# Optimization experiments

Hardware: AMD Instinct MI355X
Metric: run time of the kernel (lower is better)

Reference implementation:

```python
import jax, jax.numpy as jnp
import numpy as np

N, E, DIN, DH, DOUT = 100000, 600000, 128, 128, 64


def _glorot(k, shape):
    lim = float(np.sqrt(6.0 / (shape[0] + shape[1])))
    return jax.random.uniform(k, shape, jnp.float32, -lim, lim)


def setup_inputs() -> dict:
    key = jax.random.key(0)
    ks = jax.random.split(key, 12)
    return {
        "x": jax.random.normal(ks[0], (N, DIN), jnp.float32),
        "src": jax.random.randint(ks[1], (E,), 0, N),
        "dst": jax.random.randint(ks[2], (E,), 0, N),
        # layer 0: NGNN_SAGEConv = SAGEConv(in,hid) + fc(hid,hid) + fc2(hid,hid)
        "w_self0": _glorot(ks[3], (DIN, DH)), "b_self0": jnp.zeros((DH,), jnp.float32),
        "w_neigh0": _glorot(ks[4], (DIN, DH)),
        "fc_w": _glorot(ks[5], (DH, DH)), "fc_b": jnp.zeros((DH,), jnp.float32),
        "fc2_w": _glorot(ks[6], (DH, DH)), "fc2_b": jnp.zeros((DH,), jnp.float32),
        # layer 1: SAGEConv(hid,hid)
        "w_self1": _glorot(ks[7], (DH, DH)), "b_self1": jnp.zeros((DH,), jnp.float32),
        "w_neigh1": _glorot(ks[8], (DH, DH)),
        # layer 2: SAGEConv(hid,out)
        "w_self2": _glorot(ks[9], (DH, DOUT)), "b_self2": jnp.zeros((DOUT,), jnp.float32),
        "w_neigh2": _glorot(ks[10], (DH, DOUT)),
    }


def _sage_conv(x, src, dst, w_self, b_self, w_neigh):
    # DGL SAGEConv, aggregator='mean': out = x @ W_self + b + mean_{u->v} x_u @ W_neigh
    agg = jax.ops.segment_sum(x[src], dst, num_segments=N)          # [N, d_in]
    deg = jax.ops.segment_sum(jnp.ones((src.shape[0],), x.dtype), dst, num_segments=N)
    h_neigh = agg / jnp.maximum(deg, 1.0)[:, None]                  # zero-in-degree -> 0
    return x @ w_self + b_self + h_neigh @ w_neigh


def reference(x, src, dst,
              w_self0, b_self0, w_neigh0, fc_w, fc_b, fc2_w, fc2_b,
              w_self1, b_self1, w_neigh1,
              w_self2, b_self2, w_neigh2):
    # layer 0: NGNN_SAGEConv with num_nonl_layers=2, then outer ReLU (dropout: eval = identity)
    h = _sage_conv(x, src, dst, w_self0, b_self0, w_neigh0)
    h = jax.nn.relu(h)
    h = h @ fc_w + fc_b
    h = jax.nn.relu(h)
    h = h @ fc2_w + fc2_b
    h = jax.nn.relu(h)
    # layer 1: SAGEConv + ReLU
    h = _sage_conv(h, src, dst, w_self1, b_self1, w_neigh1)
    h = jax.nn.relu(h)
    # layer 2 (output): SAGEConv, no activation
    return _sage_conv(h, src, dst, w_self2, b_self2, w_neigh2)
```

## Files before the change

kernel.cpp:

```cpp
#include <hip/hip_runtime.h>

#define N_NODES 100000
#define N_EDGES 600000
#define K_DIM   128
#define NPART   ((N_NODES + 255) / 256)

typedef unsigned short ushort_t;
typedef short v8s __attribute__((ext_vector_type(8)));
typedef float v4f __attribute__((ext_vector_type(4)));

__device__ __forceinline__ ushort_t f2b(float f) {
  unsigned u = __builtin_bit_cast(unsigned, f);
  unsigned r = u + 0x7FFFu + ((u >> 16) & 1u);
  return (ushort_t)(r >> 16);
}
__device__ __forceinline__ float b2f(ushort_t h) {
  return __builtin_bit_cast(float, (unsigned)h << 16);
}
__device__ __forceinline__ float blo(unsigned u) {
  return __builtin_bit_cast(float, u << 16);
}
__device__ __forceinline__ float bhi(unsigned u) {
  return __builtin_bit_cast(float, u & 0xFFFF0000u);
}


__global__ void deg_kernel(const int* __restrict__ dst, int* __restrict__ deg) {
  int e = blockIdx.x * blockDim.x + threadIdx.x;
  if (e < N_EDGES) atomicAdd(&deg[dst[e]], 1);
}

__global__ void scan1_kernel(const int* __restrict__ deg, int* __restrict__ excl,
                             int* __restrict__ partials) {
  __shared__ int s[256];
  int t = threadIdx.x, i = blockIdx.x * 256 + t;
  int v = (i < N_NODES) ? deg[i] : 0;
  s[t] = v;
  __syncthreads();
  for (int off = 1; off < 256; off <<= 1) {
    int x = (t >= off) ? s[t - off] : 0;
    __syncthreads();
    s[t] += x;
    __syncthreads();
  }
  if (i < N_NODES) excl[i] = s[t] - v;
  if (t == 255) partials[blockIdx.x] = s[t];
}

__global__ void scan2_kernel(int* __restrict__ partials) {
  __shared__ int s[512];
  int t = threadIdx.x;
  int v = (t < NPART) ? partials[t] : 0;
  s[t] = v;
  __syncthreads();
  for (int off = 1; off < 512; off <<= 1) {
    int x = (t >= off) ? s[t - off] : 0;
    __syncthreads();
    s[t] += x;
    __syncthreads();
  }
  if (t < NPART) partials[t] = s[t] - v;
}

__global__ void scan3_kernel(const int* __restrict__ excl, const int* __restrict__ partials,
                             const int* __restrict__ deg, int* __restrict__ row_ptr,
                             int* __restrict__ cursor, float* __restrict__ inv_deg) {
  int i = blockIdx.x * blockDim.x + threadIdx.x;
  if (i < N_NODES) {
    int rp = excl[i] + partials[i >> 8];
    row_ptr[i] = rp;
    cursor[i] = rp;
    inv_deg[i] = 1.0f / (float)(deg[i] > 1 ? deg[i] : 1);
  } else if (i == N_NODES) {
    row_ptr[N_NODES] = N_EDGES;
  }
}

__global__ void fill_kernel(const int* __restrict__ src, const int* __restrict__ dst,
                            int* __restrict__ cursor, int* __restrict__ ssrc) {
  int e = blockIdx.x * blockDim.x + threadIdx.x;
  if (e < N_EDGES) {
    int p = atomicAdd(&cursor[dst[e]], 1);
    ssrc[p] = src[e];
  }
}


__global__ void cast_kernel(const float* __restrict__ X, ushort_t* __restrict__ Xb) {
  int i = (blockIdx.x * 256 + threadIdx.x) * 4;
  if (i >= N_NODES * K_DIM) return;
  float4 v = *(const float4*)(X + i);
  ushort4 h;
  h.x = f2b(v.x); h.y = f2b(v.y); h.z = f2b(v.z); h.w = f2b(v.w);
  *(ushort4*)(Xb + i) = h;
}

__global__ void swizzle_all_kernel(
    const float* __restrict__ w0, const float* __restrict__ w1,
    const float* __restrict__ w2, const float* __restrict__ w3,
    const float* __restrict__ w4, const float* __restrict__ w5,
    const float* __restrict__ w6, const float* __restrict__ w7,
    ushort_t* __restrict__ s0, ushort_t* __restrict__ s1,
    ushort_t* __restrict__ s2, ushort_t* __restrict__ s3,
    ushort_t* __restrict__ s4, ushort_t* __restrict__ s5,
    ushort_t* __restrict__ s6, ushort_t* __restrict__ s7) {
  const int z = blockIdx.z;
  const float* W;
  ushort_t* S;
  int dout = 128;
  switch (z) {
    case 0: W = w0; S = s0; break;
    case 1: W = w1; S = s1; break;
    case 2: W = w2; S = s2; break;
    case 3: W = w3; S = s3; break;
    case 4: W = w4; S = s4; break;
    case 5: W = w5; S = s5; break;
    case 6: W = w6; S = s6; dout = 64; break;
    default: W = w7; S = s7; dout = 64; break;
  }
  int t = blockIdx.x * 256 + threadIdx.x;
  if (t >= K_DIM * dout) return;
  int k = t / dout, n = t % dout;
  S[(k >> 3) * (dout * 8) + n * 8 + (k & 7)] = f2b(W[t]);
}


__global__ __launch_bounds__(256, 8) void agg_kernel(
    const ushort_t* __restrict__ Hh,
    const int* __restrict__ row_ptr, const int* __restrict__ ssrc,
    const float* __restrict__ inv_deg, ushort_t* __restrict__ Ah) {
  const int tid = threadIdx.x;
  const int c0  = (tid & 7) * 16;
  const int r   = tid >> 3;
  const int v   = blockIdx.x * 32 + r;
  if (v >= N_NODES) return;

  float a[16];
  #pragma unroll
  for (int i = 0; i < 16; ++i) a[i] = 0.f;

  const int beg = row_ptr[v], end = row_ptr[v + 1];
  int e = beg;
  for (; e + 2 <= end; e += 2) {
    const size_t r0 = (size_t)ssrc[e] * K_DIM + c0;
    const size_t r1 = (size_t)ssrc[e + 1] * K_DIM + c0;
    const uint4 p0 = *(const uint4*)(Hh + r0);
    const uint4 p1 = *(const uint4*)(Hh + r0 + 8);
    const uint4 q0 = *(const uint4*)(Hh + r1);
    const uint4 q1 = *(const uint4*)(Hh + r1 + 8);
    a[ 0] += blo(p0.x) + blo(q0.x);  a[ 1] += bhi(p0.x) + bhi(q0.x);
    a[ 2] += blo(p0.y) + blo(q0.y);  a[ 3] += bhi(p0.y) + bhi(q0.y);
    a[ 4] += blo(p0.z) + blo(q0.z);  a[ 5] += bhi(p0.z) + bhi(q0.z);
    a[ 6] += blo(p0.w) + blo(q0.w);  a[ 7] += bhi(p0.w) + bhi(q0.w);
    a[ 8] += blo(p1.x) + blo(q1.x);  a[ 9] += bhi(p1.x) + bhi(q1.x);
    a[10] += blo(p1.y) + blo(q1.y);  a[11] += bhi(p1.y) + bhi(q1.y);
    a[12] += blo(p1.z) + blo(q1.z);  a[13] += bhi(p1.z) + bhi(q1.z);
    a[14] += blo(p1.w) + blo(q1.w);  a[15] += bhi(p1.w) + bhi(q1.w);
  }
  if (e < end) {
    const size_t r0 = (size_t)ssrc[e] * K_DIM + c0;
    const uint4 p0 = *(const uint4*)(Hh + r0);
    const uint4 p1 = *(const uint4*)(Hh + r0 + 8);
    a[ 0] += blo(p0.x);  a[ 1] += bhi(p0.x);
    a[ 2] += blo(p0.y);  a[ 3] += bhi(p0.y);
    a[ 4] += blo(p0.z);  a[ 5] += bhi(p0.z);
    a[ 6] += blo(p0.w);  a[ 7] += bhi(p0.w);
    a[ 8] += blo(p1.x);  a[ 9] += bhi(p1.x);
    a[10] += blo(p1.y);  a[11] += bhi(p1.y);
    a[12] += blo(p1.z);  a[13] += bhi(p1.z);
    a[14] += blo(p1.w);  a[15] += bhi(p1.w);
  }
  const float sc = inv_deg[v];
  const size_t wo = (size_t)v * K_DIM + c0;
  #pragma unroll
  for (int g = 0; g < 4; ++g) {
    ushort4 oh;
    oh.x = f2b(a[4 * g + 0] * sc);
    oh.y = f2b(a[4 * g + 1] * sc);
    oh.z = f2b(a[4 * g + 2] * sc);
    oh.w = f2b(a[4 * g + 3] * sc);
    *(ushort4*)(Ah + wo + 4 * g) = oh;
  }
}


template <int DOUT_FULL, bool TWO, bool RELU, bool BF16_OUT>
__global__ __launch_bounds__(256, 4) void mfma_gemm_kernel(
    const ushort_t* __restrict__ A1, const ushort_t* __restrict__ A2,
    const ushort_t* __restrict__ W1sw, const ushort_t* __restrict__ W2sw,
    const float* __restrict__ bias,
    ushort_t* __restrict__ Obf, float* __restrict__ Ofp) {
  constexpr int COLT = 64;
  constexpr int NT   = COLT / 16;
  constexpr int SWN  = (K_DIM / 8) * COLT * 8;
  __shared__ ushort_t sW[SWN];

  const int tid  = threadIdx.x;
  const int wv   = tid >> 6;
  const int lane = tid & 63;
  const int lm   = lane & 15;
  const int q    = lane >> 4;
  const int row0 = blockIdx.x * 128 + wv * 32;
  const int col0 = blockIdx.y * COLT;

  for (int i = tid * 8; i < SWN; i += 2048) {
    const int kg = i / (COLT * 8);
    const int nl = (i >> 3) & (COLT - 1);
    *(uint4*)&sW[i] = *(const uint4*)&W1sw[kg * (DOUT_FULL * 8) + (col0 + nl) * 8];
  }
  __syncthreads();

  int ra = row0 + lm;       ra = ra < N_NODES ? ra : N_NODES - 1;
  int rb = row0 + 16 + lm;  rb = rb < N_NODES ? rb : N_NODES - 1;
  const size_t off0 = (size_t)ra * K_DIM;
  const size_t off1 = (size_t)rb * K_DIM;

  v4f acc[2][NT];
  #pragma unroll
  for (int m = 0; m < 2; ++m)
    #pragma unroll
    for (int n = 0; n < NT; ++n) acc[m][n] = (v4f){0.f, 0.f, 0.f, 0.f};

  for (int ks = 0; ks < K_DIM / 32; ++ks) {
    const int ko = ks * 32 + q * 8;
    const v8s a0 = *(const v8s*)(A1 + off0 + ko);
    const v8s a1 = *(const v8s*)(A1 + off1 + ko);
    #pragma unroll
    for (int nt = 0; nt < NT; ++nt) {
      const v8s b = *(const v8s*)&sW[((ks * 4 + q) * COLT + nt * 16 + lm) * 8];
      acc[0][nt] = __builtin_amdgcn_mfma_f32_16x16x32_bf16(a0, b, acc[0][nt], 0, 0, 0);
      acc[1][nt] = __builtin_amdgcn_mfma_f32_16x16x32_bf16(a1, b, acc[1][nt], 0, 0, 0);
    }
  }

  if (TWO) {
    __syncthreads();
    for (int i = tid * 8; i < SWN; i += 2048) {
      const int kg = i / (COLT * 8);
      const int nl = (i >> 3) & (COLT - 1);
      *(uint4*)&sW[i] = *(const uint4*)&W2sw[kg * (DOUT_FULL * 8) + (col0 + nl) * 8];
    }
    __syncthreads();

    for (int ks = 0; ks < K_DIM / 32; ++ks) {
      const int ko = ks * 32 + q * 8;
      const v8s a0 = *(const v8s*)(A2 + off0 + ko);
      const v8s a1 = *(const v8s*)(A2 + off1 + ko);
      #pragma unroll
      for (int nt = 0; nt < NT; ++nt) {
        const v8s b = *(const v8s*)&sW[((ks * 4 + q) * COLT + nt * 16 + lm) * 8];
        acc[0][nt] = __builtin_amdgcn_mfma_f32_16x16x32_bf16(a0, b, acc[0][nt], 0, 0, 0);
        acc[1][nt] = __builtin_amdgcn_mfma_f32_16x16x32_bf16(a1, b, acc[1][nt], 0, 0, 0);
      }
    }
  }

  #pragma unroll
  for (int m = 0; m < 2; ++m) {
    #pragma unroll
    for (int nt = 0; nt < NT; ++nt) {
      const int col = col0 + nt * 16 + lm;
      const float bv = bias[col];
      #pragma unroll
      for (int r = 0; r < 4; ++r) {
        const int row = row0 + m * 16 + q * 4 + r;
        if (row < N_NODES) {
          float v = acc[m][nt][r] + bv;
          if (RELU) v = v > 0.f ? v : 0.f;
          if (BF16_OUT) Obf[(size_t)row * DOUT_FULL + col] = f2b(v);
          else          Ofp[(size_t)row * DOUT_FULL + col] = v;
        }
      }
    }
  }
}


__global__ __launch_bounds__(256, 2) void fused_fc_kernel(
    const ushort_t* __restrict__ A,
    const ushort_t* __restrict__ W1sw, const ushort_t* __restrict__ W2sw,
    const float* __restrict__ b1, const float* __restrict__ b2,
    ushort_t* __restrict__ O) {
  constexpr int NT = 8;
  constexpr int HP = 136;
  __shared__ ushort_t bufW[K_DIM * 128];
  __shared__ ushort_t bufH[128 * HP];

  const int tid   = threadIdx.x;
  const int wv    = tid >> 6;
  const int lane  = tid & 63;
  const int lm    = lane & 15;
  const int q     = lane >> 4;
  const int lrow0 = wv * 32;
  const int row0  = blockIdx.x * 128 + lrow0;

  for (int i = tid * 8; i < K_DIM * 128; i += 2048)
    *(uint4*)&bufW[i] = *(const uint4*)&W1sw[i];
  __syncthreads();

  int ra = row0 + lm;       ra = ra < N_NODES ? ra : N_NODES - 1;
  int rb = row0 + 16 + lm;  rb = rb < N_NODES ? rb : N_NODES - 1;
  const size_t off0 = (size_t)ra * K_DIM;
  const size_t off1 = (size_t)rb * K_DIM;

  v4f acc[2][NT];
  #pragma unroll
  for (int m = 0; m < 2; ++m)
    #pragma unroll
    for (int n = 0; n < NT; ++n) acc[m][n] = (v4f){0.f, 0.f, 0.f, 0.f};

  for (int ks = 0; ks < K_DIM / 32; ++ks) {
    const int ko = ks * 32 + q * 8;
    const v8s a0 = *(const v8s*)(A + off0 + ko);
    const v8s a1 = *(const v8s*)(A + off1 + ko);
    #pragma unroll
    for (int nt = 0; nt < NT; ++nt) {
      const v8s b = *(const v8s*)&bufW[((ks * 4 + q) * 128 + nt * 16 + lm) * 8];
      acc[0][nt] = __builtin_amdgcn_mfma_f32_16x16x32_bf16(a0, b, acc[0][nt], 0, 0, 0);
      acc[1][nt] = __builtin_amdgcn_mfma_f32_16x16x32_bf16(a1, b, acc[1][nt], 0, 0, 0);
    }
  }
  __syncthreads();

  #pragma unroll
  for (int m = 0; m < 2; ++m) {
    #pragma unroll
    for (int nt = 0; nt < NT; ++nt) {
      const int col = nt * 16 + lm;
      const float bv = b1[col];
      #pragma unroll
      for (int r = 0; r < 4; ++r) {
        float v = acc[m][nt][r] + bv;
        v = v > 0.f ? v : 0.f;
        bufH[(lrow0 + m * 16 + q * 4 + r) * HP + col] = f2b(v);
        acc[m][nt][r] = 0.f;
      }
    }
  }
  for (int i = tid * 8; i < K_DIM * 128; i += 2048)
    *(uint4*)&bufW[i] = *(const uint4*)&W2sw[i];
  __syncthreads();

  for (int ks = 0; ks < K_DIM / 32; ++ks) {
    const int ko = ks * 32 + q * 8;
    const v8s a0 = *(const v8s*)&bufH[(lrow0 + lm) * HP + ko];
    const v8s a1 = *(const v8s*)&bufH[(lrow0 + 16 + lm) * HP + ko];
    #pragma unroll
    for (int nt = 0; nt < NT; ++nt) {
      const v8s b = *(const v8s*)&bufW[((ks * 4 + q) * 128 + nt * 16 + lm) * 8];
      acc[0][nt] = __builtin_amdgcn_mfma_f32_16x16x32_bf16(a0, b, acc[0][nt], 0, 0, 0);
      acc[1][nt] = __builtin_amdgcn_mfma_f32_16x16x32_bf16(a1, b, acc[1][nt], 0, 0, 0);
    }
  }

  #pragma unroll
  for (int m = 0; m < 2; ++m) {
    #pragma unroll
    for (int nt = 0; nt < NT; ++nt) {
      const int col = nt * 16 + lm;
      const float bv = b2[col];
      #pragma unroll
      for (int r = 0; r < 4; ++r) {
        const int row = row0 + m * 16 + q * 4 + r;
        if (row < N_NODES) {
          float v = acc[m][nt][r] + bv;
          v = v > 0.f ? v : 0.f;
          O[(size_t)row * 128 + col] = f2b(v);
        }
      }
    }
  }
}


extern "C" void kernel_launch(void* const* d_in, const int* in_sizes, int n_in,
                              void* d_out, int out_size, void* d_ws, size_t ws_size,
                              hipStream_t stream) {
  const float* x        = (const float*)d_in[0];
  const int*   src      = (const int*)d_in[1];
  const int*   dst      = (const int*)d_in[2];
  const float* w_self0  = (const float*)d_in[3];
  const float* b_self0  = (const float*)d_in[4];
  const float* w_neigh0 = (const float*)d_in[5];
  const float* fc_w     = (const float*)d_in[6];
  const float* fc_b     = (const float*)d_in[7];
  const float* fc2_w    = (const float*)d_in[8];
  const float* fc2_b    = (const float*)d_in[9];
  const float* w_self1  = (const float*)d_in[10];
  const float* b_self1  = (const float*)d_in[11];
  const float* w_neigh1 = (const float*)d_in[12];
  const float* w_self2  = (const float*)d_in[13];
  const float* b_self2  = (const float*)d_in[14];
  const float* w_neigh2 = (const float*)d_in[15];

  char* p = (char*)d_ws;
  auto carve = [&](size_t bytes) {
    void* q = (void*)p;
    p += (bytes + 511) & ~(size_t)511;
    return q;
  };
  const size_t PLANE = (size_t)N_NODES * K_DIM * sizeof(ushort_t);
  ushort_t* X   = (ushort_t*)carve(PLANE);
  ushort_t* Y   = (ushort_t*)carve(PLANE);
  ushort_t* Z   = (ushort_t*)carve(PLANE);
  ushort_t* ws0 = (ushort_t*)carve(K_DIM * 128 * 2);
  ushort_t* wn0 = (ushort_t*)carve(K_DIM * 128 * 2);
  ushort_t* wfc = (ushort_t*)carve(K_DIM * 128 * 2);
  ushort_t* wf2 = (ushort_t*)carve(K_DIM * 128 * 2);
  ushort_t* ws1 = (ushort_t*)carve(K_DIM * 128 * 2);
  ushort_t* wn1 = (ushort_t*)carve(K_DIM * 128 * 2);
  ushort_t* ws2 = (ushort_t*)carve(K_DIM * 64 * 2);
  ushort_t* wn2 = (ushort_t*)carve(K_DIM * 64 * 2);
  int*   ssrc    = (int*)carve((size_t)N_EDGES * 4);
  int*   row_ptr = (int*)carve((size_t)(N_NODES + 1) * 4);
  int*   cursor  = (int*)carve((size_t)N_NODES * 4);
  int*   deg     = (int*)carve((size_t)N_NODES * 4);
  int*   excl    = (int*)carve((size_t)N_NODES * 4);
  int*   parts   = (int*)carve(512 * 4);
  float* inv_deg = (float*)carve((size_t)N_NODES * 4);

  hipMemsetAsync(deg, 0, (size_t)N_NODES * 4, stream);
  const int EB = (N_EDGES + 255) / 256;
  deg_kernel<<<EB, 256, 0, stream>>>(dst, deg);
  scan1_kernel<<<NPART, 256, 0, stream>>>(deg, excl, parts);
  scan2_kernel<<<1, 512, 0, stream>>>(parts);
  scan3_kernel<<<((N_NODES + 1) + 255) / 256, 256, 0, stream>>>(excl, parts, deg,
                                                                row_ptr, cursor, inv_deg);
  fill_kernel<<<EB, 256, 0, stream>>>(src, dst, cursor, ssrc);

  cast_kernel<<<(N_NODES * K_DIM / 4 + 255) / 256, 256, 0, stream>>>(x, X);
  swizzle_all_kernel<<<dim3(64, 1, 8), 256, 0, stream>>>(
      w_self0, w_neigh0, fc_w, fc2_w, w_self1, w_neigh1, w_self2, w_neigh2,
      ws0, wn0, wfc, wf2, ws1, wn1, ws2, wn2);

  const int AB = (N_NODES + 31) / 32;
  const int GB = (N_NODES + 127) / 128;
  const dim3 G2(GB, 2), G1(GB, 1);

  agg_kernel<<<AB, 256, 0, stream>>>(X, row_ptr, ssrc, inv_deg, Y);
  mfma_gemm_kernel<128, true, true, true><<<G2, 256, 0, stream>>>(
      X, Y, ws0, wn0, b_self0, Z, nullptr);
  fused_fc_kernel<<<G1, 256, 0, stream>>>(Z, wfc, wf2, fc_b, fc2_b, Y);
  agg_kernel<<<AB, 256, 0, stream>>>(Y, row_ptr, ssrc, inv_deg, X);
  mfma_gemm_kernel<128, true, true, true><<<G2, 256, 0, stream>>>(
      Y, X, ws1, wn1, b_self1, Z, nullptr);
  agg_kernel<<<AB, 256, 0, stream>>>(Z, row_ptr, ssrc, inv_deg, Y);
  mfma_gemm_kernel<64, true, false, false><<<G1, 256, 0, stream>>>(
      Z, Y, ws2, wn2, b_self2, nullptr, (float*)d_out);
}
```

Measured before the change: 368.4 us.

## Read GEMM weights straight from global memory and merge the cast and swizzle kernels

Removes the shared-memory staging of swizzled weights in the MFMA GEMM and fused FC kernels. Weight fragments are now loaded directly from global memory, where they should mostly hit in cache, and the __syncthreads barriers that guarded the staging are gone. Launch-bounds occupancy hints are raised to match the smaller LDS footprint. The input cast and weight swizzle kernels are also combined into a single launch; the risk is more global and L2 traffic for each weight fragment.

```diff
diff --git a/kernel.cpp b/kernel.cpp
--- a/kernel.cpp
+++ b/kernel.cpp
@@ -4,6 +4,7 @@
 #define N_EDGES 600000
 #define K_DIM   128
 #define NPART   ((N_NODES + 255) / 256)
+#define CAST_BLOCKS (N_NODES * K_DIM / 4 / 256)
 
 typedef unsigned short ushort_t;
 typedef short v8s __attribute__((ext_vector_type(8)));
@@ -86,16 +87,8 @@
 }
 
 
-__global__ void cast_kernel(const float* __restrict__ X, ushort_t* __restrict__ Xb) {
-  int i = (blockIdx.x * 256 + threadIdx.x) * 4;
-  if (i >= N_NODES * K_DIM) return;
-  float4 v = *(const float4*)(X + i);
-  ushort4 h;
-  h.x = f2b(v.x); h.y = f2b(v.y); h.z = f2b(v.z); h.w = f2b(v.w);
-  *(ushort4*)(Xb + i) = h;
-}
-
-__global__ void swizzle_all_kernel(
+__global__ void prep_kernel(
+    const float* __restrict__ x, ushort_t* __restrict__ Xb,
     const float* __restrict__ w0, const float* __restrict__ w1,
     const float* __restrict__ w2, const float* __restrict__ w3,
     const float* __restrict__ w4, const float* __restrict__ w5,
@@ -104,7 +97,17 @@
     ushort_t* __restrict__ s2, ushort_t* __restrict__ s3,
     ushort_t* __restrict__ s4, ushort_t* __restrict__ s5,
     ushort_t* __restrict__ s6, ushort_t* __restrict__ s7) {
-  const int z = blockIdx.z;
+  const int b = blockIdx.x;
+  if (b < CAST_BLOCKS) {
+    int i = (b * 256 + threadIdx.x) * 4;
+    float4 v = *(const float4*)(x + i);
+    ushort4 h;
+    h.x = f2b(v.x); h.y = f2b(v.y); h.z = f2b(v.z); h.w = f2b(v.w);
+    *(ushort4*)(Xb + i) = h;
+    return;
+  }
+  const int zz = b - CAST_BLOCKS;
+  const int z  = zz >> 6;
   const float* W;
   ushort_t* S;
   int dout = 128;
@@ -118,7 +121,7 @@
     case 6: W = w6; S = s6; dout = 64; break;
     default: W = w7; S = s7; dout = 64; break;
   }
-  int t = blockIdx.x * 256 + threadIdx.x;
+  int t = (zz & 63) * 256 + threadIdx.x;
   if (t >= K_DIM * dout) return;
   int k = t / dout, n = t % dout;
   S[(k >> 3) * (dout * 8) + n * 8 + (k & 7)] = f2b(W[t]);
@@ -185,15 +188,13 @@
 
 
 template <int DOUT_FULL, bool TWO, bool RELU, bool BF16_OUT>
-__global__ __launch_bounds__(256, 4) void mfma_gemm_kernel(
+__global__ __launch_bounds__(256, 6) void mfma_gemm_kernel(
     const ushort_t* __restrict__ A1, const ushort_t* __restrict__ A2,
     const ushort_t* __restrict__ W1sw, const ushort_t* __restrict__ W2sw,
     const float* __restrict__ bias,
     ushort_t* __restrict__ Obf, float* __restrict__ Ofp) {
   constexpr int COLT = 64;
   constexpr int NT   = COLT / 16;
-  constexpr int SWN  = (K_DIM / 8) * COLT * 8;
-  __shared__ ushort_t sW[SWN];
 
   const int tid  = threadIdx.x;
   const int wv   = tid >> 6;
@@ -203,13 +204,6 @@
   const int row0 = blockIdx.x * 128 + wv * 32;
   const int col0 = blockIdx.y * COLT;
 
-  for (int i = tid * 8; i < SWN; i += 2048) {
-    const int kg = i / (COLT * 8);
-    const int nl = (i >> 3) & (COLT - 1);
-    *(uint4*)&sW[i] = *(const uint4*)&W1sw[kg * (DOUT_FULL * 8) + (col0 + nl) * 8];
-  }
-  __syncthreads();
-
   int ra = row0 + lm;       ra = ra < N_NODES ? ra : N_NODES - 1;
   int rb = row0 + 16 + lm;  rb = rb < N_NODES ? rb : N_NODES - 1;
   const size_t off0 = (size_t)ra * K_DIM;
@@ -225,30 +219,24 @@
     const int ko = ks * 32 + q * 8;
     const v8s a0 = *(const v8s*)(A1 + off0 + ko);
     const v8s a1 = *(const v8s*)(A1 + off1 + ko);
-    #pragma unroll
-    for (int nt = 0; nt < NT; ++nt) {
-      const v8s b = *(const v8s*)&sW[((ks * 4 + q) * COLT + nt * 16 + lm) * 8];
+    const ushort_t* wb = W1sw + (size_t)(ks * 4 + q) * (DOUT_FULL * 8) + (col0 + lm) * 8;
+    #pragma unroll
+    for (int nt = 0; nt < NT; ++nt) {
+      const v8s b = *(const v8s*)(wb + nt * 128);
       acc[0][nt] = __builtin_amdgcn_mfma_f32_16x16x32_bf16(a0, b, acc[0][nt], 0, 0, 0);
       acc[1][nt] = __builtin_amdgcn_mfma_f32_16x16x32_bf16(a1, b, acc[1][nt], 0, 0, 0);
     }
   }
 
   if (TWO) {
-    __syncthreads();
-    for (int i = tid * 8; i < SWN; i += 2048) {
-      const int kg = i / (COLT * 8);
-      const int nl = (i >> 3) & (COLT - 1);
-      *(uint4*)&sW[i] = *(const uint4*)&W2sw[kg * (DOUT_FULL * 8) + (col0 + nl) * 8];
-    }
-    __syncthreads();
-
     for (int ks = 0; ks < K_DIM / 32; ++ks) {
       const int ko = ks * 32 + q * 8;
       const v8s a0 = *(const v8s*)(A2 + off0 + ko);
       const v8s a1 = *(const v8s*)(A2 + off1 + ko);
+      const ushort_t* wb = W2sw + (size_t)(ks * 4 + q) * (DOUT_FULL * 8) + (col0 + lm) * 8;
       #pragma unroll
       for (int nt = 0; nt < NT; ++nt) {
-        const v8s b = *(const v8s*)&sW[((ks * 4 + q) * COLT + nt * 16 + lm) * 8];
+        const v8s b = *(const v8s*)(wb + nt * 128);
         acc[0][nt] = __builtin_amdgcn_mfma_f32_16x16x32_bf16(a0, b, acc[0][nt], 0, 0, 0);
         acc[1][nt] = __builtin_amdgcn_mfma_f32_16x16x32_bf16(a1, b, acc[1][nt], 0, 0, 0);
       }
@@ -276,14 +264,13 @@
 }
 
 
-__global__ __launch_bounds__(256, 2) void fused_fc_kernel(
+__global__ __launch_bounds__(256, 4) void fused_fc_kernel(
     const ushort_t* __restrict__ A,
     const ushort_t* __restrict__ W1sw, const ushort_t* __restrict__ W2sw,
     const float* __restrict__ b1, const float* __restrict__ b2,
     ushort_t* __restrict__ O) {
   constexpr int NT = 8;
   constexpr int HP = 136;
-  __shared__ ushort_t bufW[K_DIM * 128];
   __shared__ ushort_t bufH[128 * HP];
 
   const int tid   = threadIdx.x;
@@ -294,10 +281,6 @@
   const int lrow0 = wv * 32;
   const int row0  = blockIdx.x * 128 + lrow0;
 
-  for (int i = tid * 8; i < K_DIM * 128; i += 2048)
-    *(uint4*)&bufW[i] = *(const uint4*)&W1sw[i];
-  __syncthreads();
-
   int ra = row0 + lm;       ra = ra < N_NODES ? ra : N_NODES - 1;
   int rb = row0 + 16 + lm;  rb = rb < N_NODES ? rb : N_NODES - 1;
   const size_t off0 = (size_t)ra * K_DIM;
@@ -313,14 +296,14 @@
     const int ko = ks * 32 + q * 8;
     const v8s a0 = *(const v8s*)(A + off0 + ko);
     const v8s a1 = *(const v8s*)(A + off1 + ko);
-    #pragma unroll
-    for (int nt = 0; nt < NT; ++nt) {
-      const v8s b = *(const v8s*)&bufW[((ks * 4 + q) * 128 + nt * 16 + lm) * 8];
+    const ushort_t* wb = W1sw + (size_t)(ks * 4 + q) * (128 * 8) + lm * 8;
+    #pragma unroll
+    for (int nt = 0; nt < NT; ++nt) {
+      const v8s b = *(const v8s*)(wb + nt * 128);
       acc[0][nt] = __builtin_amdgcn_mfma_f32_16x16x32_bf16(a0, b, acc[0][nt], 0, 0, 0);
       acc[1][nt] = __builtin_amdgcn_mfma_f32_16x16x32_bf16(a1, b, acc[1][nt], 0, 0, 0);
     }
   }
-  __syncthreads();
 
   #pragma unroll
   for (int m = 0; m < 2; ++m) {
@@ -337,17 +320,15 @@
       }
     }
   }
-  for (int i = tid * 8; i < K_DIM * 128; i += 2048)
-    *(uint4*)&bufW[i] = *(const uint4*)&W2sw[i];
-  __syncthreads();
 
   for (int ks = 0; ks < K_DIM / 32; ++ks) {
     const int ko = ks * 32 + q * 8;
     const v8s a0 = *(const v8s*)&bufH[(lrow0 + lm) * HP + ko];
     const v8s a1 = *(const v8s*)&bufH[(lrow0 + 16 + lm) * HP + ko];
-    #pragma unroll
-    for (int nt = 0; nt < NT; ++nt) {
-      const v8s b = *(const v8s*)&bufW[((ks * 4 + q) * 128 + nt * 16 + lm) * 8];
+    const ushort_t* wb = W2sw + (size_t)(ks * 4 + q) * (128 * 8) + lm * 8;
+    #pragma unroll
+    for (int nt = 0; nt < NT; ++nt) {
+      const v8s b = *(const v8s*)(wb + nt * 128);
       acc[0][nt] = __builtin_amdgcn_mfma_f32_16x16x32_bf16(a0, b, acc[0][nt], 0, 0, 0);
       acc[1][nt] = __builtin_amdgcn_mfma_f32_16x16x32_bf16(a1, b, acc[1][nt], 0, 0, 0);
     }
@@ -428,8 +409,8 @@
                                                                 row_ptr, cursor, inv_deg);
   fill_kernel<<<EB, 256, 0, stream>>>(src, dst, cursor, ssrc);
 
-  cast_kernel<<<(N_NODES * K_DIM / 4 + 255) / 256, 256, 0, stream>>>(x, X);
-  swizzle_all_kernel<<<dim3(64, 1, 8), 256, 0, stream>>>(
+  prep_kernel<<<CAST_BLOCKS + 512, 256, 0, stream>>>(
+      x, X,
       w_self0, w_neigh0, fc_w, fc2_w, w_self1, w_neigh1, w_self2, w_neigh2,
       ws0, wn0, wfc, wf2, ws1, wn1, ws2, wn2);
 
```

Measured after the change: 391.0 us. +6.1%, slower.
